# Performance work log

Hardware: AMD Instinct MI355X
Metric: run time of the kernel (lower is better)

## Reference

```python
import jax, jax.numpy as jnp
import numpy as np

S = 1024      # MAX_SEQ_LEN
D_IN = 4096
H = 32        # num_heads
G = 8         # num_kv_groups
HD = 128      # head_dim
GS = H // G   # group_size


def _rope(t, cos, sin):
    # t: [heads, S, HD]; cos/sin: [S, HD]
    half = HD // 2
    t1, t2 = t[..., :half], t[..., half:]
    rotated = jnp.concatenate([-t2, t1], axis=-1)
    return t * cos[None] + rotated * sin[None]


def setup_inputs() -> dict:
    key = jax.random.key(0)
    ks = jax.random.split(key, 8)
    x = jax.random.normal(ks[0], (1, S, D_IN), dtype=jnp.float32)
    mask = jnp.triu(jnp.ones((S, S), dtype=bool), k=1)  # causal: True above diagonal
    # RoPE tables (standard llama frequencies)
    inv_freq = 1.0 / (10000.0 ** (jnp.arange(0, HD, 2, dtype=jnp.float32) / HD))
    angles = jnp.arange(S, dtype=jnp.float32)[:, None] * inv_freq[None, :]  # [S, HD/2]
    angles = jnp.concatenate([angles, angles], axis=-1)                     # [S, HD]
    cos, sin = jnp.cos(angles), jnp.sin(angles)
    sc = 0.02
    Wq = jax.random.normal(ks[1], (D_IN, H * HD), dtype=jnp.float32) * sc
    Wk = jax.random.normal(ks[2], (D_IN, G * HD), dtype=jnp.float32) * sc
    Wv = jax.random.normal(ks[3], (D_IN, G * HD), dtype=jnp.float32) * sc
    Wo = jax.random.normal(ks[4], (H * HD, D_IN), dtype=jnp.float32) * sc
    return {"x": x, "mask": mask, "cos": cos, "sin": sin,
            "Wq": Wq, "Wk": Wk, "Wv": Wv, "Wo": Wo}


def reference(x, mask, cos, sin, Wq, Wk, Wv, Wo):
    b, n_tok, _ = x.shape  # b == 1 (module squeezes dim 0)
    xs = x[0]                                        # [S, d_in]
    q = (xs @ Wq).reshape(n_tok, H, HD).transpose(1, 0, 2)   # [H, S, HD]
    k = (xs @ Wk).reshape(n_tok, G, HD).transpose(1, 0, 2)   # [G, S, HD]
    v = (xs @ Wv).reshape(n_tok, G, HD).transpose(1, 0, 2)   # [G, S, HD]
    q = _rope(q, cos, sin)
    k = _rope(k, cos, sin)
    # GQA expansion: repeat_interleave over head dim
    k = jnp.repeat(k, GS, axis=0)                    # [H, S, HD]
    v = jnp.repeat(v, GS, axis=0)
    scores = jnp.einsum('hsd,htd->hst', q, k)        # [H, S, S]
    scores = jnp.where(mask[None], -jnp.inf, scores) / jnp.sqrt(jnp.float32(HD))
    weights = jax.nn.softmax(scores, axis=-1)
    ctx = jnp.einsum('hst,htd->hsd', weights, v)     # [H, S, HD]
    ctx = ctx.transpose(1, 0, 2).reshape(n_tok, H * HD)
    out = ctx @ Wo                                   # [S, d_in]
    return out[None]                                 # [1, S, d_in]
```

## Files before the change

kernel.cpp:

```cpp
#include <hip/hip_runtime.h>
#include <hip/hip_bf16.h>

#define S_LEN 1024
#define DIN 4096
#define NH 32
#define NG 8
#define HD 128

typedef __bf16 bf16x8 __attribute__((ext_vector_type(8)));
typedef __bf16 bf16x4 __attribute__((ext_vector_type(4)));
typedef float f32x4 __attribute__((ext_vector_type(4)));

__device__ __forceinline__ void gload_lds16(const void* g, void* l) {
  __builtin_amdgcn_global_load_lds(
      (const __attribute__((address_space(1))) unsigned int*)g,
      (__attribute__((address_space(3))) unsigned int*)l, 16, 0, 0);
}

__device__ __forceinline__ unsigned pack2bf(float a, float b) {
  union { __bf16 h[2]; unsigned u; } x;
  x.h[0] = (__bf16)a; x.h[1] = (__bf16)b;
  return x.u;
}

__global__ __launch_bounds__(256) void k_cast(const float* __restrict__ in,
                                              __bf16* __restrict__ out, int n4) {
  int i = blockIdx.x * 256 + threadIdx.x;
  if (i >= n4) return;
  const float4 v = ((const float4*)in)[i];
  bf16x4 o;
  o.x = (__bf16)v.x; o.y = (__bf16)v.y; o.z = (__bf16)v.z; o.w = (__bf16)v.w;
  ((bf16x4*)out)[i] = o;
}

__global__ __launch_bounds__(256) void k_transpose_cast(const float* __restrict__ W,
                                                        __bf16* __restrict__ WT,
                                                        int N, int K) {
  __shared__ __bf16 t[64][80];
  const int tid = threadIdx.x;
  const int k0 = blockIdx.y * 64, n0 = blockIdx.x * 64;
#pragma unroll
  for (int p = 0; p < 4; ++p) {
    int kk = p * 16 + (tid >> 4);
    int nn = (tid & 15) * 4;
    const float4 v = *(const float4*)&W[(size_t)(k0 + kk) * N + n0 + nn];
    t[nn + 0][kk] = (__bf16)v.x;
    t[nn + 1][kk] = (__bf16)v.y;
    t[nn + 2][kk] = (__bf16)v.z;
    t[nn + 3][kk] = (__bf16)v.w;
  }
  __syncthreads();
#pragma unroll
  for (int p = 0; p < 2; ++p) {
    int nn = p * 32 + (tid >> 3);
    int kk = (tid & 7) * 8;
    bf16x8 v = *(const bf16x8*)&t[nn][kk];
    *(bf16x8*)&WT[(size_t)(n0 + nn) * K + k0 + kk] = v;
  }
}

__global__ __launch_bounds__(256) void k_rope(__bf16* __restrict__ Q, __bf16* __restrict__ Kb,
                                              const float* __restrict__ cosT,
                                              const float* __restrict__ sinT) {
  int idx = blockIdx.x * 256 + threadIdx.x;
  const int QP = S_LEN * NH * 64;
  __bf16* t; int nh;
  if (idx < QP) { t = Q; nh = NH; }
  else {
    idx -= QP; t = Kb; nh = NG;
    if (idx >= S_LEN * NG * 64) return;
  }
  int d = idx & 63;
  int h = (idx >> 6) % nh;
  int s = idx / (64 * nh);
  float c = cosT[s * HD + d], sn = sinT[s * HD + d];
  size_t base = (size_t)s * nh * HD + h * HD + d;
  float t1 = (float)t[base], t2 = (float)t[base + 64];
  t[base]      = (__bf16)(t1 * c - t2 * sn);
  t[base + 64] = (__bf16)(t2 * c + t1 * sn);
}

__global__ __launch_bounds__(256) void k_vt(const __bf16* __restrict__ V,
                                            __bf16* __restrict__ Vt) {
  __shared__ __bf16 t[64][72];
  const int tid = threadIdx.x;
  const int s0 = blockIdx.y * 64, d0 = blockIdx.x * 64;
#pragma unroll
  for (int p = 0; p < 2; ++p) {
    int ss = p * 32 + (tid >> 3);
    int dd = (tid & 7) * 8;
    bf16x8 v = *(const bf16x8*)&V[(size_t)(s0 + ss) * 1024 + d0 + dd];
#pragma unroll
    for (int e = 0; e < 8; ++e) t[dd + e][ss] = v[e];
  }
  __syncthreads();
#pragma unroll
  for (int p = 0; p < 2; ++p) {
    int dd = p * 32 + (tid >> 3);
    int ss = (tid & 7) * 8;
    *(bf16x8*)&Vt[(size_t)(d0 + dd) * 1024 + s0 + ss] = *(const bf16x8*)&t[dd][ss];
  }
}

template <int MODE, typename OutT>
__global__ __launch_bounds__(256, 3) void k_gemm(const __bf16* __restrict__ A,
                                                 const __bf16* __restrict__ Bt,
                                                 OutT* __restrict__ C, int N, int K,
                                                 __bf16* __restrict__ Qb,
                                                 __bf16* __restrict__ Kb,
                                                 __bf16* __restrict__ Vb) {
  __shared__ __bf16 As[128 * 64], Bs[64 * 64];
  const int bm = blockIdx.y, bn = blockIdx.x;
  const int tid = threadIdx.x, w = tid >> 6;
  const int l = tid & 63, l15 = l & 15, g4 = l >> 4;

  f32x4 acc[2][4];
#pragma unroll
  for (int i = 0; i < 2; ++i)
#pragma unroll
    for (int j = 0; j < 4; ++j)
#pragma unroll
      for (int r = 0; r < 4; ++r) acc[i][j][r] = 0.f;

  for (int k0 = 0; k0 < K; k0 += 64) {
#pragma unroll
    for (int p = 0; p < 4; ++p) {
      int c = p * 256 + tid;
      int row = c >> 3, gc = (c & 7) ^ (row & 7);
      gload_lds16(&A[(size_t)(bm * 128 + row) * K + k0 + gc * 8], &As[(p * 256 + w * 64) * 8]);
    }
#pragma unroll
    for (int p = 0; p < 2; ++p) {
      int c = p * 256 + tid;
      int row = c >> 3, gc = (c & 7) ^ (row & 7);
      gload_lds16(&Bt[(size_t)(bn * 64 + row) * K + k0 + gc * 8], &Bs[(p * 256 + w * 64) * 8]);
    }
    __syncthreads();

    bf16x8 af[2][2], bfr[4][2];
#pragma unroll
    for (int i = 0; i < 2; ++i) {
      int m = w * 32 + i * 16 + l15;
#pragma unroll
      for (int kk = 0; kk < 2; ++kk)
        af[i][kk] = *(const bf16x8*)((const char*)As + m * 128 + (((kk * 4 + g4) ^ (m & 7)) << 4));
    }
#pragma unroll
    for (int j = 0; j < 4; ++j) {
      int n = j * 16 + l15;
#pragma unroll
      for (int kk = 0; kk < 2; ++kk)
        bfr[j][kk] = *(const bf16x8*)((const char*)Bs + n * 128 + (((kk * 4 + g4) ^ (n & 7)) << 4));
    }
#pragma unroll
    for (int kk = 0; kk < 2; ++kk)
#pragma unroll
      for (int i = 0; i < 2; ++i)
#pragma unroll
        for (int j = 0; j < 4; ++j)
          acc[i][j] = __builtin_amdgcn_mfma_f32_16x16x32_bf16(af[i][kk], bfr[j][kk], acc[i][j], 0, 0, 0);
    __syncthreads();
  }

  if constexpr (MODE == 0) {
#pragma unroll
    for (int i = 0; i < 2; ++i)
#pragma unroll
      for (int j = 0; j < 4; ++j)
#pragma unroll
        for (int r = 0; r < 4; ++r) {
          size_t row = bm * 128 + w * 32 + i * 16 + g4 * 4 + r;
          size_t col = bn * 64 + j * 16 + l15;
          C[row * N + col] = (OutT)acc[i][j][r];
        }
  } else {
    const int nb0 = bn * 64;
    __bf16* dst; int ldc, coff;
    if (nb0 < 4096)      { dst = Qb; ldc = 4096; coff = 0; }
    else if (nb0 < 5120) { dst = Kb; ldc = 1024; coff = 4096; }
    else                 { dst = Vb; ldc = 1024; coff = 5120; }
#pragma unroll
    for (int i = 0; i < 2; ++i)
#pragma unroll
      for (int j = 0; j < 4; ++j)
#pragma unroll
        for (int r = 0; r < 4; ++r) {
          size_t row = bm * 128 + w * 32 + i * 16 + g4 * 4 + r;
          size_t col = nb0 + j * 16 + l15 - coff;
          dst[row * ldc + col] = (__bf16)acc[i][j][r];
        }
  }
}

__global__ __launch_bounds__(256) void k_attn(const __bf16* __restrict__ Q,
                                              const __bf16* __restrict__ Kb,
                                              const __bf16* __restrict__ Vt,
                                              __bf16* __restrict__ ctx) {
  __shared__ __align__(16) char lds_raw[65536];
  __bf16* Ks = (__bf16*)lds_raw;
  __bf16* Vs = (__bf16*)(lds_raw + 32768);

  const int h = blockIdx.y, g = h >> 2;
  const int q0 = blockIdx.x * 64;
  const int tid = threadIdx.x, w = tid >> 6, l = tid & 63;
  const int l15 = l & 15, g4 = l >> 4;
  const float scale = 0.08838834764831845f;

  bf16x8 qf[4];
  const int qrow = q0 + w * 16 + l15;
#pragma unroll
  for (int ks = 0; ks < 4; ++ks)
    qf[ks] = *(const bf16x8*)&Q[(size_t)qrow * (NH * HD) + h * HD + ks * 32 + g4 * 8];

  f32x4 acc[8];
#pragma unroll
  for (int i = 0; i < 8; ++i)
#pragma unroll
    for (int r = 0; r < 4; ++r) acc[i][r] = 0.f;
  float m_run = -__builtin_inff(), l_run = 0.f;

  const int ntiles = (q0 + 64 + 127) >> 7;
  for (int kt = 0; kt < ntiles; ++kt) {
    const int kv0 = kt * 128;
#pragma unroll
    for (int p = 0; p < 8; ++p) {
      int c = p * 256 + tid;
      int row = c >> 4, cc = c & 15;
      gload_lds16(&Kb[(size_t)(kv0 + row) * (NG * HD) + g * HD + ((cc ^ (row & 7)) << 3)],
                  &Ks[(p * 256 + w * 64) * 8]);
      gload_lds16(&Vt[(size_t)(g * HD + row) * S_LEN + kv0 + ((cc ^ (row & 7)) << 3)],
                  &Vs[(p * 256 + w * 64) * 8]);
    }
    __syncthreads();

    float sreg[8][4];
    const bool need_mask = (kv0 + 127 > q0);
#pragma unroll
    for (int tf = 0; tf < 8; ++tf) {
      f32x4 sa;
#pragma unroll
      for (int r = 0; r < 4; ++r) sa[r] = 0.f;
      int t_loc = tf * 16 + l15;
#pragma unroll
      for (int ks = 0; ks < 4; ++ks) {
        bf16x8 kf = *(const bf16x8*)((const char*)Ks + t_loc * 256 + (((ks * 4 + g4) ^ (t_loc & 7)) << 4));
        sa = __builtin_amdgcn_mfma_f32_16x16x32_bf16(kf, qf[ks], sa, 0, 0, 0);
      }
#pragma unroll
      for (int r = 0; r < 4; ++r) {
        float v = sa[r] * scale;
        if (need_mask && (kv0 + tf * 16 + g4 * 4 + r) > qrow) v = -__builtin_inff();
        sreg[tf][r] = v;
      }
    }
    float mx = -__builtin_inff();
#pragma unroll
    for (int tf = 0; tf < 8; ++tf)
#pragma unroll
      for (int r = 0; r < 4; ++r) mx = fmaxf(mx, sreg[tf][r]);
    mx = fmaxf(mx, __shfl_xor(mx, 16));
    mx = fmaxf(mx, __shfl_xor(mx, 32));
    const float m_new = fmaxf(m_run, mx);
    const float alpha = __expf(m_run - m_new);
    float ssum = 0.f;
#pragma unroll
    for (int tf = 0; tf < 8; ++tf)
#pragma unroll
      for (int r = 0; r < 4; ++r) {
        sreg[tf][r] = __expf(sreg[tf][r] - m_new);
        ssum += sreg[tf][r];
      }
    ssum += __shfl_xor(ssum, 16);
    ssum += __shfl_xor(ssum, 32);
    l_run = l_run * alpha + ssum;
    m_run = m_new;
    float ar[4];
#pragma unroll
    for (int r = 0; r < 4; ++r) ar[r] = __shfl(alpha, g4 * 4 + r);
#pragma unroll
    for (int nf = 0; nf < 8; ++nf)
#pragma unroll
      for (int r = 0; r < 4; ++r) acc[nf][r] *= ar[r];

    __syncthreads();

    char* pb = lds_raw + w * 4096;
#pragma unroll
    for (int tf = 0; tf < 8; ++tf) {
      int chunkc = 2 * tf + (g4 >> 1);
      int addr = l15 * 256 + ((chunkc ^ (l15 & 7)) << 4) + ((g4 & 1) << 3);
      *(unsigned*)(pb + addr)     = pack2bf(sreg[tf][0], sreg[tf][1]);
      *(unsigned*)(pb + addr + 4) = pack2bf(sreg[tf][2], sreg[tf][3]);
    }
    asm volatile("s_waitcnt lgkmcnt(0)" ::: "memory");
    bf16x8 pf[4];
#pragma unroll
    for (int ks = 0; ks < 4; ++ks)
      pf[ks] = *(const bf16x8*)(pb + l15 * 256 + (((ks * 4 + g4) ^ (l15 & 7)) << 4));
#pragma unroll
    for (int nf = 0; nf < 8; ++nf) {
      int d_loc = nf * 16 + l15;
#pragma unroll
      for (int ks = 0; ks < 4; ++ks) {
        bf16x8 vf = *(const bf16x8*)((const char*)Vs + d_loc * 256 + (((ks * 4 + g4) ^ (d_loc & 7)) << 4));
        acc[nf] = __builtin_amdgcn_mfma_f32_16x16x32_bf16(pf[ks], vf, acc[nf], 0, 0, 0);
      }
    }
    __syncthreads();
  }
  float li[4];
#pragma unroll
  for (int r = 0; r < 4; ++r) li[r] = 1.f / __shfl(l_run, g4 * 4 + r);
#pragma unroll
  for (int nf = 0; nf < 8; ++nf)
#pragma unroll
    for (int r = 0; r < 4; ++r) {
      size_t row = q0 + w * 16 + g4 * 4 + r;
      size_t col = (size_t)h * HD + nf * 16 + l15;
      ctx[row * (NH * HD) + col] = (__bf16)(acc[nf][r] * li[r]);
    }
}

extern "C" void kernel_launch(void* const* d_in, const int* in_sizes, int n_in,
                              void* d_out, int out_size, void* d_ws, size_t ws_size,
                              hipStream_t stream) {
  const float* x    = (const float*)d_in[0];
  const float* cosT = (const float*)d_in[2];
  const float* sinT = (const float*)d_in[3];
  const float* Wq   = (const float*)d_in[4];
  const float* Wk   = (const float*)d_in[5];
  const float* Wv   = (const float*)d_in[6];
  const float* Wo   = (const float*)d_in[7];
  float* out = (float*)d_out;

  char* ws = (char*)d_ws;
  const size_t MB = 1u << 20;
  __bf16* xb    = (__bf16*)(ws + 0);
  __bf16* WqkvT = (__bf16*)(ws + 8 * MB);
  __bf16* WoT   = (__bf16*)(ws + 56 * MB);
  __bf16* Qb    = (__bf16*)(ws + 88 * MB);
  __bf16* Kbuf  = (__bf16*)(ws + 96 * MB);
  __bf16* Vb    = (__bf16*)(ws + 98 * MB);
  __bf16* Vtb   = (__bf16*)(ws + 100 * MB);
  __bf16* ctxb  = (__bf16*)(ws + 0);

  k_cast<<<4096, 256, 0, stream>>>(x, xb, (S_LEN * DIN) / 4);
  k_transpose_cast<<<dim3(64, 64), 256, 0, stream>>>(Wq, WqkvT, 4096, 4096);
  k_transpose_cast<<<dim3(16, 64), 256, 0, stream>>>(Wk, WqkvT + (size_t)4096 * 4096, 1024, 4096);
  k_transpose_cast<<<dim3(16, 64), 256, 0, stream>>>(Wv, WqkvT + (size_t)5120 * 4096, 1024, 4096);
  k_transpose_cast<<<dim3(64, 64), 256, 0, stream>>>(Wo, WoT, 4096, 4096);

  k_gemm<1, __bf16><<<dim3(96, 8), 256, 0, stream>>>(xb, WqkvT, (__bf16*)nullptr, 6144, 4096,
                                                     Qb, Kbuf, Vb);
  k_rope<<<10240, 256, 0, stream>>>(Qb, Kbuf, cosT, sinT);
  k_vt<<<dim3(16, 16), 256, 0, stream>>>(Vb, Vtb);

  k_attn<<<dim3(16, 32), 256, 0, stream>>>(Qb, Kbuf, Vtb, ctxb);

  k_gemm<0, float><<<dim3(64, 8), 256, 0, stream>>>(ctxb, WoT, out, 4096, 4096,
                                                    nullptr, nullptr, nullptr);
}
```

Measured before the change: 223.2 us.

## Fuse weight transpose-cast into GEMM loads and write V transposed in epilogue

Drops the separate transpose-cast kernels for all four weight matrices and the V-transpose kernel. The GEMM now reads fp32 weights directly, packs pairs of k-rows into bf16 in registers, and stores them in a swizzled k-pair LDS layout. It double-buffers both A and B tiles so the next loads overlap the current MFMAs. The QKV GEMM epilogue writes V straight into its transposed layout. This removes a full fp32 read plus bf16 write and re-read of roughly 64M weight elements, but each GEMM tile now reads fp32 weights (twice the bytes per B tile) and uses more LDS and registers.

```diff
diff --git a/kernel.cpp b/kernel.cpp
--- a/kernel.cpp
+++ b/kernel.cpp
@@ -31,32 +31,6 @@
   bf16x4 o;
   o.x = (__bf16)v.x; o.y = (__bf16)v.y; o.z = (__bf16)v.z; o.w = (__bf16)v.w;
   ((bf16x4*)out)[i] = o;
-}
-
-__global__ __launch_bounds__(256) void k_transpose_cast(const float* __restrict__ W,
-                                                        __bf16* __restrict__ WT,
-                                                        int N, int K) {
-  __shared__ __bf16 t[64][80];
-  const int tid = threadIdx.x;
-  const int k0 = blockIdx.y * 64, n0 = blockIdx.x * 64;
-#pragma unroll
-  for (int p = 0; p < 4; ++p) {
-    int kk = p * 16 + (tid >> 4);
-    int nn = (tid & 15) * 4;
-    const float4 v = *(const float4*)&W[(size_t)(k0 + kk) * N + n0 + nn];
-    t[nn + 0][kk] = (__bf16)v.x;
-    t[nn + 1][kk] = (__bf16)v.y;
-    t[nn + 2][kk] = (__bf16)v.z;
-    t[nn + 3][kk] = (__bf16)v.w;
-  }
-  __syncthreads();
-#pragma unroll
-  for (int p = 0; p < 2; ++p) {
-    int nn = p * 32 + (tid >> 3);
-    int kk = (tid & 7) * 8;
-    bf16x8 v = *(const bf16x8*)&t[nn][kk];
-    *(bf16x8*)&WT[(size_t)(n0 + nn) * K + k0 + kk] = v;
-  }
 }
 
 __global__ __launch_bounds__(256) void k_rope(__bf16* __restrict__ Q, __bf16* __restrict__ Kb,
@@ -80,37 +54,28 @@
   t[base + 64] = (__bf16)(t2 * c + t1 * sn);
 }
 
-__global__ __launch_bounds__(256) void k_vt(const __bf16* __restrict__ V,
-                                            __bf16* __restrict__ Vt) {
-  __shared__ __bf16 t[64][72];
-  const int tid = threadIdx.x;
-  const int s0 = blockIdx.y * 64, d0 = blockIdx.x * 64;
-#pragma unroll
-  for (int p = 0; p < 2; ++p) {
-    int ss = p * 32 + (tid >> 3);
-    int dd = (tid & 7) * 8;
-    bf16x8 v = *(const bf16x8*)&V[(size_t)(s0 + ss) * 1024 + d0 + dd];
-#pragma unroll
-    for (int e = 0; e < 8; ++e) t[dd + e][ss] = v[e];
-  }
-  __syncthreads();
-#pragma unroll
-  for (int p = 0; p < 2; ++p) {
-    int dd = p * 32 + (tid >> 3);
-    int ss = (tid & 7) * 8;
-    *(bf16x8*)&Vt[(size_t)(d0 + dd) * 1024 + s0 + ss] = *(const bf16x8*)&t[dd][ss];
-  }
-}
-
-template <int MODE, typename OutT>
+template <int MODE>
 __global__ __launch_bounds__(256, 3) void k_gemm(const __bf16* __restrict__ A,
-                                                 const __bf16* __restrict__ Bt,
-                                                 OutT* __restrict__ C, int N, int K,
+                                                 const float* __restrict__ W0,
+                                                 const float* __restrict__ W1,
+                                                 const float* __restrict__ W2,
+                                                 float* __restrict__ C,
                                                  __bf16* __restrict__ Qb,
                                                  __bf16* __restrict__ Kb,
-                                                 __bf16* __restrict__ Vb) {
-  __shared__ __bf16 As[128 * 64], Bs[64 * 64];
+                                                 __bf16* __restrict__ Vt) {
+  __shared__ __bf16 As[2][128 * 64];
+  __shared__ unsigned Bs[2][32 * 64];
   const int bm = blockIdx.y, bn = blockIdx.x;
+  const int K = DIN, NT = K / 64;
+
+  const float* Wsrc; int ldb, nloc;
+  if (MODE == 0) { Wsrc = W0; ldb = 4096; nloc = bn * 64; }
+  else {
+    if (bn < 64)      { Wsrc = W0; ldb = 4096; nloc = bn * 64; }
+    else if (bn < 80) { Wsrc = W1; ldb = 1024; nloc = (bn - 64) * 64; }
+    else              { Wsrc = W2; ldb = 1024; nloc = (bn - 80) * 64; }
+  }
+
   const int tid = threadIdx.x, w = tid >> 6;
   const int l = tid & 63, l15 = l & 15, g4 = l >> 4;
 
@@ -122,44 +87,82 @@
 #pragma unroll
       for (int r = 0; r < 4; ++r) acc[i][j][r] = 0.f;
 
-  for (int k0 = 0; k0 < K; k0 += 64) {
+  float4 breg[2][2];
+
+  auto issueB = [&](int t) {
+#pragma unroll
+    for (int p = 0; p < 2; ++p) {
+      int c = p * 256 + tid;
+      int kp = c >> 4, nn = (c & 15) * 4;
+      const float* src = Wsrc + (size_t)(t * 64 + 2 * kp) * ldb + nloc + nn;
+      breg[p][0] = *(const float4*)src;
+      breg[p][1] = *(const float4*)(src + ldb);
+    }
+  };
+  auto writeB = [&](int buf) {
+#pragma unroll
+    for (int p = 0; p < 2; ++p) {
+      int c = p * 256 + tid;
+      int kp = c >> 4, nn = (c & 15) * 4;
+      int col = nn ^ (((kp >> 2) & 3) << 3);
+      uint4 d;
+      d.x = pack2bf(breg[p][0].x, breg[p][1].x);
+      d.y = pack2bf(breg[p][0].y, breg[p][1].y);
+      d.z = pack2bf(breg[p][0].z, breg[p][1].z);
+      d.w = pack2bf(breg[p][0].w, breg[p][1].w);
+      *(uint4*)&Bs[buf][kp * 64 + col] = d;
+    }
+  };
+  auto issueA = [&](int t, int buf) {
+    const __bf16* Ab = A + (size_t)(bm * 128) * K + t * 64;
 #pragma unroll
     for (int p = 0; p < 4; ++p) {
       int c = p * 256 + tid;
       int row = c >> 3, gc = (c & 7) ^ (row & 7);
-      gload_lds16(&A[(size_t)(bm * 128 + row) * K + k0 + gc * 8], &As[(p * 256 + w * 64) * 8]);
-    }
-#pragma unroll
-    for (int p = 0; p < 2; ++p) {
-      int c = p * 256 + tid;
-      int row = c >> 3, gc = (c & 7) ^ (row & 7);
-      gload_lds16(&Bt[(size_t)(bn * 64 + row) * K + k0 + gc * 8], &Bs[(p * 256 + w * 64) * 8]);
-    }
-    __syncthreads();
-
-    bf16x8 af[2][2], bfr[4][2];
+      gload_lds16(Ab + (size_t)row * K + gc * 8, &As[buf][(p * 256 + w * 64) * 8]);
+    }
+  };
+
+  issueB(0);
+  issueA(0, 0);
+  writeB(0);
+  __syncthreads();
+
+  for (int t = 0; t < NT; ++t) {
+    const int cur = t & 1;
+    if (t + 1 < NT) {
+      issueB(t + 1);
+      issueA(t + 1, cur ^ 1);
+    }
+    bf16x8 af[2][2];
 #pragma unroll
     for (int i = 0; i < 2; ++i) {
       int m = w * 32 + i * 16 + l15;
 #pragma unroll
       for (int kk = 0; kk < 2; ++kk)
-        af[i][kk] = *(const bf16x8*)((const char*)As + m * 128 + (((kk * 4 + g4) ^ (m & 7)) << 4));
-    }
-#pragma unroll
-    for (int j = 0; j < 4; ++j) {
-      int n = j * 16 + l15;
-#pragma unroll
-      for (int kk = 0; kk < 2; ++kk)
-        bfr[j][kk] = *(const bf16x8*)((const char*)Bs + n * 128 + (((kk * 4 + g4) ^ (n & 7)) << 4));
-    }
-#pragma unroll
-    for (int kk = 0; kk < 2; ++kk)
+        af[i][kk] = *(const bf16x8*)((const char*)As[cur] + m * 128 + (((kk * 4 + g4) ^ (m & 7)) << 4));
+    }
+#pragma unroll
+    for (int kk = 0; kk < 2; ++kk) {
+      union { unsigned u[4]; bf16x8 v; } fb[4];
+#pragma unroll
+      for (int j = 0; j < 4; ++j) {
+        const unsigned* bp = &Bs[cur][(kk * 16 + 4 * g4) * 64 + ((j * 16 + l15) ^ (g4 << 3))];
+        fb[j].u[0] = bp[0];
+        fb[j].u[1] = bp[64];
+        fb[j].u[2] = bp[128];
+        fb[j].u[3] = bp[192];
+      }
 #pragma unroll
       for (int i = 0; i < 2; ++i)
 #pragma unroll
         for (int j = 0; j < 4; ++j)
-          acc[i][j] = __builtin_amdgcn_mfma_f32_16x16x32_bf16(af[i][kk], bfr[j][kk], acc[i][j], 0, 0, 0);
-    __syncthreads();
+          acc[i][j] = __builtin_amdgcn_mfma_f32_16x16x32_bf16(af[i][kk], fb[j].v, acc[i][j], 0, 0, 0);
+    }
+    if (t + 1 < NT) {
+      writeB(cur ^ 1);
+      __syncthreads();
+    }
   }
 
   if constexpr (MODE == 0) {
@@ -171,24 +174,35 @@
         for (int r = 0; r < 4; ++r) {
           size_t row = bm * 128 + w * 32 + i * 16 + g4 * 4 + r;
           size_t col = bn * 64 + j * 16 + l15;
-          C[row * N + col] = (OutT)acc[i][j][r];
+          C[row * 4096 + col] = acc[i][j][r];
         }
   } else {
-    const int nb0 = bn * 64;
-    __bf16* dst; int ldc, coff;
-    if (nb0 < 4096)      { dst = Qb; ldc = 4096; coff = 0; }
-    else if (nb0 < 5120) { dst = Kb; ldc = 1024; coff = 4096; }
-    else                 { dst = Vb; ldc = 1024; coff = 5120; }
-#pragma unroll
-    for (int i = 0; i < 2; ++i)
-#pragma unroll
-      for (int j = 0; j < 4; ++j)
-#pragma unroll
-        for (int r = 0; r < 4; ++r) {
-          size_t row = bm * 128 + w * 32 + i * 16 + g4 * 4 + r;
-          size_t col = nb0 + j * 16 + l15 - coff;
-          dst[row * ldc + col] = (__bf16)acc[i][j][r];
+    if (bn < 80) {
+      __bf16* dst = (bn < 64) ? Qb : Kb;
+      int ldc = (bn < 64) ? 4096 : 1024;
+#pragma unroll
+      for (int i = 0; i < 2; ++i)
+#pragma unroll
+        for (int j = 0; j < 4; ++j)
+#pragma unroll
+          for (int r = 0; r < 4; ++r) {
+            size_t row = bm * 128 + w * 32 + i * 16 + g4 * 4 + r;
+            size_t col = nloc + j * 16 + l15;
+            dst[row * ldc + col] = (__bf16)acc[i][j][r];
+          }
+    } else {
+#pragma unroll
+      for (int i = 0; i < 2; ++i)
+#pragma unroll
+        for (int j = 0; j < 4; ++j) {
+          size_t n = nloc + j * 16 + l15;
+          size_t m0 = bm * 128 + w * 32 + i * 16 + g4 * 4;
+          bf16x4 v;
+          v.x = (__bf16)acc[i][j][0]; v.y = (__bf16)acc[i][j][1];
+          v.z = (__bf16)acc[i][j][2]; v.w = (__bf16)acc[i][j][3];
+          *(bf16x4*)&Vt[n * 1024 + m0] = v;
         }
+    }
   }
 }
 
@@ -335,28 +349,20 @@
 
   char* ws = (char*)d_ws;
   const size_t MB = 1u << 20;
-  __bf16* xb    = (__bf16*)(ws + 0);
-  __bf16* WqkvT = (__bf16*)(ws + 8 * MB);
-  __bf16* WoT   = (__bf16*)(ws + 56 * MB);
-  __bf16* Qb    = (__bf16*)(ws + 88 * MB);
-  __bf16* Kbuf  = (__bf16*)(ws + 96 * MB);
-  __bf16* Vb    = (__bf16*)(ws + 98 * MB);
-  __bf16* Vtb   = (__bf16*)(ws + 100 * MB);
-  __bf16* ctxb  = (__bf16*)(ws + 0);
+  __bf16* xb   = (__bf16*)(ws + 0);
+  __bf16* Qb   = (__bf16*)(ws + 8 * MB);
+  __bf16* Kbuf = (__bf16*)(ws + 16 * MB);
+  __bf16* Vtb  = (__bf16*)(ws + 18 * MB);
+  __bf16* ctxb = (__bf16*)(ws + 0);
 
   k_cast<<<4096, 256, 0, stream>>>(x, xb, (S_LEN * DIN) / 4);
-  k_transpose_cast<<<dim3(64, 64), 256, 0, stream>>>(Wq, WqkvT, 4096, 4096);
-  k_transpose_cast<<<dim3(16, 64), 256, 0, stream>>>(Wk, WqkvT + (size_t)4096 * 4096, 1024, 4096);
-  k_transpose_cast<<<dim3(16, 64), 256, 0, stream>>>(Wv, WqkvT + (size_t)5120 * 4096, 1024, 4096);
-  k_transpose_cast<<<dim3(64, 64), 256, 0, stream>>>(Wo, WoT, 4096, 4096);
-
-  k_gemm<1, __bf16><<<dim3(96, 8), 256, 0, stream>>>(xb, WqkvT, (__bf16*)nullptr, 6144, 4096,
-                                                     Qb, Kbuf, Vb);
+
+  k_gemm<1><<<dim3(96, 8), 256, 0, stream>>>(xb, Wq, Wk, Wv, nullptr, Qb, Kbuf, Vtb);
+
   k_rope<<<10240, 256, 0, stream>>>(Qb, Kbuf, cosT, sinT);
-  k_vt<<<dim3(16, 16), 256, 0, stream>>>(Vb, Vtb);
 
   k_attn<<<dim3(16, 32), 256, 0, stream>>>(Qb, Kbuf, Vtb, ctxb);
 
-  k_gemm<0, float><<<dim3(64, 8), 256, 0, stream>>>(ctxb, WoT, out, 4096, 4096,
-                                                    nullptr, nullptr, nullptr);
-}
+  k_gemm<0><<<dim3(64, 8), 256, 0, stream>>>(ctxb, Wo, nullptr, nullptr, out,
+                                             nullptr, nullptr, nullptr);
+}
```

Result: slower. 228.6 us (+2.4%).
